# Performance work log

Measured on AMD Instinct MI355X. Metric: run time of the kernel, lower is better.

## Reference

```python
import jax, jax.numpy as jnp
import numpy as np

N, T, H, D = 512, 256, 512, 9  # batch, decode steps, hidden, feature dim


def setup_inputs() -> dict:
    key = jax.random.key(0)
    ks = jax.random.split(key, 4)
    s = 1.0 / np.sqrt(H)
    return {
        "x": jax.random.normal(ks[0], (N, T + 1, D), dtype=jnp.float32),
        "W_ih": jax.random.normal(ks[1], (4 * H, D), dtype=jnp.float32) * s,
        "W_hh": jax.random.normal(ks[2], (4 * H, H), dtype=jnp.float32) * s,
        "b_ih": jnp.zeros((4 * H,), dtype=jnp.float32),
        "b_hh": jnp.zeros((4 * H,), dtype=jnp.float32),
        "fc_W": jax.random.normal(ks[3], (D, H), dtype=jnp.float32) * s,
        "fc_b": jnp.zeros((D,), dtype=jnp.float32),
        "h0": jnp.zeros((1, H), dtype=jnp.float32),
        "c0": jnp.zeros((1, H), dtype=jnp.float32),
    }


def _lstm_cell(x_proj, h, c, W_hh, b_hh):
    # x_proj = x @ W_ih.T + b_ih, precomputed. PyTorch LSTMCell gate order: i, f, g, o
    gates = x_proj + h @ W_hh.T + b_hh
    i, f, g, o = jnp.split(gates, 4, axis=-1)
    c_new = jax.nn.sigmoid(f) * c + jax.nn.sigmoid(i) * jnp.tanh(g)
    h_new = jax.nn.sigmoid(o) * jnp.tanh(c_new)
    return h_new, c_new


def reference(x, W_ih, W_hh, b_ih, b_hh, fc_W, fc_b, h0, c0):
    n = x.shape[0]
    h = jnp.broadcast_to(h0, (n, h0.shape[1]))
    c = jnp.broadcast_to(c0, (n, c0.shape[1]))

    # Encode phase: consume all T+1 input steps (precompute input projections in one GEMM)
    x_proj = jnp.einsum('ntd,gd->tng', x, W_ih) + b_ih  # [T+1, N, 4H]

    def enc_step(carry, xp):
        h, c = carry
        h, c = _lstm_cell(xp, h, c, W_hh, b_hh)
        return (h, c), None

    (h, c), _ = jax.lax.scan(enc_step, (h, c), x_proj)

    # Decode phase: T steps with zero input (input projection reduces to b_ih)
    zero_proj = jnp.broadcast_to(b_ih, (n, b_ih.shape[0]))

    def dec_step(carry, _):
        h, c = carry
        h, c = _lstm_cell(zero_proj, h, c, W_hh, b_hh)
        out = jax.nn.sigmoid(h @ fc_W.T + fc_b)  # [N, D]
        return (h, c), out

    n_dec = x.shape[1] - 1
    _, outs = jax.lax.scan(dec_step, (h, c), None, length=n_dec)  # [T, N, D]
    return jnp.transpose(outs, (1, 0, 2))  # [N, T, D]
```

## Files before the change

### kernel.cpp

```cpp
#include <hip/hip_runtime.h>


#define TT 256
#define HH 512
#define DD 9
#define TP1 257
#define NSTEP 513
#define THREADS 512
#define NWG 256
#define NCL 8
#define WPC 32

#define WF_HI_B 0u
#define WF_LO_B 2097152u
#define HFRAG_B 4194304u
#define U32_B   8388608u

#define L_ST    0
#define L_EX    16384
#define L_HNEW  20480
#define L_WIH   21520
#define L_MISC  22160
#define L_TOT   22164

typedef short s8v __attribute__((ext_vector_type(8)));
typedef float f4v __attribute__((ext_vector_type(4)));
typedef int   i4v __attribute__((ext_vector_type(4)));

__device__ __forceinline__ float sigmoidf_(float v){ return 1.0f/(1.0f+__expf(-v)); }
__device__ __forceinline__ float tanhf_(float v){ return 1.0f - 2.0f/(__expf(2.0f*v)+1.0f); }
__device__ __forceinline__ unsigned short bf16hi_rne(float f){
    unsigned u = __float_as_uint(f);
    return (unsigned short)((u + 0x7fffu + ((u>>16)&1u)) >> 16);
}
#define B2F_LO(u) __uint_as_float(((unsigned)(u))<<16)
#define B2F_HI(u) __uint_as_float(((unsigned)(u)) & 0xffff0000u)

__device__ __forceinline__ void ld16i(i4v& d, const char* p){
    asm volatile("global_load_dwordx4 %0, %1, off sc0" : "=v"(d) : "v"(p));
}
__device__ __forceinline__ void wait_vm0_mem(){
    asm volatile("s_waitcnt vmcnt(0)" ::: "memory");
}
__device__ __forceinline__ void wait_vm0_4i(i4v& a0,i4v& a1,i4v& a2,i4v& a3){
    asm volatile("s_waitcnt vmcnt(0)"
                 : "+v"(a0),"+v"(a1),"+v"(a2),"+v"(a3) :: "memory");
}
__device__ __forceinline__ void lgkm0_bar(){
    asm volatile("s_waitcnt lgkmcnt(0)" ::: "memory");
    __builtin_amdgcn_s_barrier();
}

__global__ void rnn_init_kernel(const float* __restrict__ W_hh,
                                const float* __restrict__ h0,
                                char* __restrict__ wsb) {
    int idx = blockIdx.x * blockDim.x + threadIdx.x;
    {
        int i  = idx & 7;
        int l  = (idx >> 3) & 63;
        int kt = (idx >> 9) & 15;
        int rb = (idx >> 13) & 3;
        int wl = idx >> 15;
        int mm = l & 15, gg = l >> 4;
        int gt = mm & 3, lu = mm >> 2;
        int grow = gt * 512 + wl * 16 + rb * 4 + lu;
        int k = kt * 32 + gg * 8 + i;
        float v = W_hh[grow * 512 + k];
        unsigned short hi = bf16hi_rne(v);
        float fh = __uint_as_float(((unsigned)hi) << 16);
        unsigned short lo = bf16hi_rne(v - fh);
        ((unsigned short*)(wsb + WF_HI_B))[idx] = hi;
        ((unsigned short*)(wsb + WF_LO_B))[idx] = lo;
    }
    if (idx < 262144) {
        int i   = idx & 7;
        int gg  = (idx >> 9) & 3;
        int kt  = (idx >> 11) & 15;
        int cl  = idx >> 15;
        int rem = idx & 32767;
        int j = kt * 32 + gg * 8 + i;
        ((unsigned short*)(wsb + HFRAG_B + (unsigned)cl * 65536u))[rem] = bf16hi_rne(h0[j]);
    }
    if (idx < 2048) ((unsigned int*)(wsb + U32_B))[idx] = 0u;
}

__global__ __attribute__((amdgpu_waves_per_eu(2, 2))) __launch_bounds__(THREADS)
void rnn_persist_kernel(const float* __restrict__ x,
                        const float* __restrict__ W_ih,
                        const float* __restrict__ b_ih,
                        const float* __restrict__ b_hh,
                        const float* __restrict__ fc_W,
                        const float* __restrict__ fc_b,
                        const float* __restrict__ c0,
                        char* __restrict__ wsb,
                        float* __restrict__ out) {
    __shared__ float smem[L_TOT];
    char* ldsst = (char*)smem;

    const int wg  = blockIdx.x;
    const int cl  = wg & 7;
    const int wl  = wg >> 3;
    const int j0  = wl * 16;
    const int nb0 = cl * 64;
    const int tid = threadIdx.x;
    const int lane = tid & 63;
    const int wid  = tid >> 6;
    const int rb   = wid & 3;
    const int kh   = wid >> 2;
    const int m    = lane & 15;
    const int g    = lane >> 4;
    const int gu   = wl * 16 + rb * 4 + g;
    const int c0i  = kh * 32 + m;

    unsigned int* flags = (unsigned int*)(wsb + U32_B);
    unsigned int* ctr   = (unsigned int*)(wsb + U32_B + 3072);
    unsigned int* xccb  = (unsigned int*)(wsb + U32_B + 4096);

    for (int i2 = tid; i2 < 16 * 36; i2 += THREADS) {
        int u = i2 / 36; int r2 = i2 - u * 36; int gt = r2 / 9; int d = r2 - gt * 9;
        smem[L_WIH + u * 40 + gt * 9 + d] = W_ih[(gt * 512 + wl * 16 + u) * DD + d];
    }

    const float bias0 = b_ih[gu]        + b_hh[gu];
    const float bias1 = b_ih[512 + gu]  + b_hh[512 + gu];
    const float bias2 = b_ih[1024 + gu] + b_hh[1024 + gu];
    const float bias3 = b_ih[1536 + gu] + b_hh[1536 + gu];
    float creg0 = c0[gu], creg1 = c0[gu];

    s8v wAh[8], wAl[8];
    {
        const char* base = wsb + (unsigned)(((wl*4 + rb)*16 + kh*8)*64 + lane)*16u;
#pragma unroll
        for (int j = 0; j < 8; ++j) {
            wAh[j] = *(const s8v*)(base + WF_HI_B + j*1024);
            wAl[j] = *(const s8v*)(base + WF_LO_B + j*1024);
        }
    }

    if (tid == 0) {
        unsigned xcc;
        asm volatile("s_getreg_b32 %0, hwreg(HW_REG_XCC_ID, 0, 32)" : "=s"(xcc));
        __hip_atomic_store(xccb + wg, xcc + 1u, __ATOMIC_RELAXED, __HIP_MEMORY_SCOPE_AGENT);
        __hip_atomic_fetch_add(ctr, 1u, __ATOMIC_RELEASE, __HIP_MEMORY_SCOPE_AGENT);
        while (__hip_atomic_load(ctr, __ATOMIC_RELAXED, __HIP_MEMORY_SCOPE_AGENT) < NWG)
            __builtin_amdgcn_s_sleep(8);
    }
    __syncthreads();
    {
        unsigned v = (tid < WPC)
            ? __hip_atomic_load(xccb + cl + 8 * tid, __ATOMIC_RELAXED,
                                __HIP_MEMORY_SCOPE_AGENT) : 0u;
        unsigned v0 = __shfl(v, 0, 64);
        bool ok = (tid >= WPC) || (v != 0u && v == v0);
        unsigned long long mk = __ballot(ok);
        if (tid == 0) smem[L_MISC] = (mk == ~0ull) ? 1.0f : 0.0f;
    }
    __syncthreads();
    const bool fast = (smem[L_MISC] != 0.0f);

    const int fg = tid >> 4, fl = tid & 15;

    for (int s = 0; s < NSTEP; ++s) {
        const int par = s & 1;
        const char* hsrc = wsb + HFRAG_B + (unsigned)(par*8 + cl) * 65536u;
        unsigned int* flg = flags + cl * 32;
        const bool dec = (s >= TP1 + 1);
        const bool enc = (s < TP1);

        if (s > 0) {
            if (tid < WPC) {
                for (;;) {
                    unsigned v = __hip_atomic_load(flg + tid, __ATOMIC_RELAXED,
                                                   __HIP_MEMORY_SCOPE_AGENT);
                    if (__all((int)(v >= (unsigned)s))) break;
                    __builtin_amdgcn_s_sleep(2);
                }
            }
            __syncthreads();
            if (fast) __builtin_amdgcn_fence(__ATOMIC_ACQUIRE, "workgroup");
            else      __builtin_amdgcn_fence(__ATOMIC_ACQUIRE, "agent");
        }

        i4v hb[4];
#pragma unroll
        for (int c = 0; c < 4; ++c)
            ld16i(hb[c], hsrc + c*8192 + tid*16);

        float xv0[DD], xv1[DD];
        if (enc) {
            const float* xp0 = x + (size_t)(nb0 + c0i) * (TP1 * DD) + s * DD;
            const float* xp1 = x + (size_t)(nb0 + c0i + 16) * (TP1 * DD) + s * DD;
#pragma unroll
            for (int d = 0; d < DD; ++d) { xv0[d] = xp0[d]; xv1[d] = xp1[d]; }
        }

        wait_vm0_mem();
#pragma unroll
        for (int c = 0; c < 4; ++c)
            *(i4v*)(ldsst + c*8192 + tid*16) = hb[c];
#pragma unroll
        for (int c = 0; c < 4; ++c)
            ld16i(hb[c], hsrc + 32768 + c*8192 + tid*16);
        lgkm0_bar();

        f4v a0 = {0,0,0,0}, a1 = {0,0,0,0}, a2 = {0,0,0,0}, a3 = {0,0,0,0};
        if (kh == 0) {
#pragma unroll
            for (int j = 0; j < 8; ++j) {
                const char* bb = ldsst + j*4096 + g*1024 + m*16;
                s8v bh0 = *(const s8v*)(bb);
                s8v bh1 = *(const s8v*)(bb + 256);
                s8v bh2 = *(const s8v*)(bb + 512);
                s8v bh3 = *(const s8v*)(bb + 768);
                a0 = __builtin_amdgcn_mfma_f32_16x16x32_bf16(wAh[j], bh0, a0, 0,0,0);
                a1 = __builtin_amdgcn_mfma_f32_16x16x32_bf16(wAh[j], bh1, a1, 0,0,0);
                a2 = __builtin_amdgcn_mfma_f32_16x16x32_bf16(wAh[j], bh2, a2, 0,0,0);
                a3 = __builtin_amdgcn_mfma_f32_16x16x32_bf16(wAh[j], bh3, a3, 0,0,0);
                a0 = __builtin_amdgcn_mfma_f32_16x16x32_bf16(wAl[j], bh0, a0, 0,0,0);
                a1 = __builtin_amdgcn_mfma_f32_16x16x32_bf16(wAl[j], bh1, a1, 0,0,0);
                a2 = __builtin_amdgcn_mfma_f32_16x16x32_bf16(wAl[j], bh2, a2, 0,0,0);
                a3 = __builtin_amdgcn_mfma_f32_16x16x32_bf16(wAl[j], bh3, a3, 0,0,0);
            }
            float* pe = smem + L_EX + ((rb*2 + 0)*64 + lane)*8;
            *(f4v*)(pe)     = a2;
            *(f4v*)(pe + 4) = a3;
        }

        wait_vm0_mem();
#pragma unroll
        for (int c = 0; c < 4; ++c)
            *(i4v*)(ldsst + 32768 + c*8192 + tid*16) = hb[c];

        i4v qa0, qa1, qa2, qa3;
        if (dec) {
            const int bselL = (fg < 2 * DD) ? (fg / DD) : 0;
            const int blL = wl * 2 + bselL;
            const char* hp = hsrc + fl*4096 + blL*16;
            ld16i(qa0, hp);          ld16i(qa1, hp + 1024);
            ld16i(qa2, hp + 2048);   ld16i(qa3, hp + 3072);
        }
        lgkm0_bar();

        if (kh == 1) {
#pragma unroll
            for (int j = 0; j < 8; ++j) {
                const char* bb = ldsst + 32768 + j*4096 + g*1024 + m*16;
                s8v bh0 = *(const s8v*)(bb);
                s8v bh1 = *(const s8v*)(bb + 256);
                s8v bh2 = *(const s8v*)(bb + 512);
                s8v bh3 = *(const s8v*)(bb + 768);
                a0 = __builtin_amdgcn_mfma_f32_16x16x32_bf16(wAh[j], bh0, a0, 0,0,0);
                a1 = __builtin_amdgcn_mfma_f32_16x16x32_bf16(wAh[j], bh1, a1, 0,0,0);
                a2 = __builtin_amdgcn_mfma_f32_16x16x32_bf16(wAh[j], bh2, a2, 0,0,0);
                a3 = __builtin_amdgcn_mfma_f32_16x16x32_bf16(wAh[j], bh3, a3, 0,0,0);
                a0 = __builtin_amdgcn_mfma_f32_16x16x32_bf16(wAl[j], bh0, a0, 0,0,0);
                a1 = __builtin_amdgcn_mfma_f32_16x16x32_bf16(wAl[j], bh1, a1, 0,0,0);
                a2 = __builtin_amdgcn_mfma_f32_16x16x32_bf16(wAl[j], bh2, a2, 0,0,0);
                a3 = __builtin_amdgcn_mfma_f32_16x16x32_bf16(wAl[j], bh3, a3, 0,0,0);
            }
            float* pe = smem + L_EX + ((rb*2 + 1)*64 + lane)*8;
            *(f4v*)(pe)     = a0;
            *(f4v*)(pe + 4) = a1;
        }
        lgkm0_bar();

        {
            const float* px = smem + L_EX + ((rb*2 + (kh^1))*64 + lane)*8;
            f4v r0 = *(const f4v*)(px);
            f4v r1 = *(const f4v*)(px + 4);
            f4v ka, kb;
            if (kh == 0) { ka = a0 + r0; kb = a1 + r1; }
            else         { ka = a2 + r0; kb = a3 + r1; }

            float s00=0,s01=0,s02=0,s03=0, s10=0,s11=0,s12=0,s13=0;
            if (enc) {
                const float* wb2 = smem + L_WIH + (rb*4 + g) * 40;
#pragma unroll
                for (int r2 = 0; r2 < 9; ++r2) {
                    f4v w4 = *(const f4v*)(wb2 + r2*4);
#pragma unroll
                    for (int e = 0; e < 4; ++e) {
                        const int fl2 = r2*4 + e;
                        const int gt = fl2 / 9, d = fl2 - gt*9;
                        const float w = w4[e];
                        const float p0 = xv0[d] * w, p1 = xv1[d] * w;
                        if (gt == 0) { s00 += p0; s10 += p1; }
                        else if (gt == 1) { s01 += p0; s11 += p1; }
                        else if (gt == 2) { s02 += p0; s12 += p1; }
                        else { s03 += p0; s13 += p1; }
                    }
                }
            }
            {
                float vi = ka.x + bias0 + s00, vf = ka.y + bias1 + s01;
                float vg = ka.z + bias2 + s02, vo = ka.w + bias3 + s03;
                float cn = sigmoidf_(vf) * creg0 + sigmoidf_(vi) * tanhf_(vg);
                creg0 = cn;
                smem[L_HNEW + (rb*4 + g) * 65 + c0i] = sigmoidf_(vo) * tanhf_(cn);
            }
            {
                float vi = kb.x + bias0 + s10, vf = kb.y + bias1 + s11;
                float vg = kb.z + bias2 + s12, vo = kb.w + bias3 + s13;
                float cn = sigmoidf_(vf) * creg1 + sigmoidf_(vi) * tanhf_(vg);
                creg1 = cn;
                smem[L_HNEW + (rb*4 + g) * 65 + c0i + 16] = sigmoidf_(vo) * tanhf_(cn);
            }
        }
        lgkm0_bar();

        if (tid < 128) {
            const int col = tid & 63, jblk = (tid >> 6) & 1;
            const int jb = wl * 2 + jblk;
            const int kt = jb >> 2, gg = jb & 3;
            s8v v;
#pragma unroll
            for (int i = 0; i < 8; ++i)
                v[i] = (short)bf16hi_rne(smem[L_HNEW + (jblk * 8 + i) * 65 + col]);
            char* dst = wsb + HFRAG_B + (unsigned)((par^1)*8 + cl)*65536u
                        + (unsigned)(kt*4096 + gg*1024 + col*16);
            *(s8v*)dst = v;
        }
        wait_vm0_mem();
        __syncthreads();

        if (tid == 0) {
            if (fast) {
                __hip_atomic_store(flg + wl, (unsigned)(s + 1),
                                   __ATOMIC_RELAXED, __HIP_MEMORY_SCOPE_AGENT);
            } else {
                __builtin_amdgcn_fence(__ATOMIC_RELEASE, "agent");
                __hip_atomic_store(flg + wl, (unsigned)(s + 1),
                                   __ATOMIC_RELEASE, __HIP_MEMORY_SCOPE_AGENT);
            }
        }

        if (dec && fg < 2 * DD) {
            const int bsel = fg / DD, d = fg - bsel * DD;
            const int bl = wl * 2 + bsel;
            const f4v* wf = (const f4v*)(fc_W + d * HH + fl * 32);
            wait_vm0_4i(qa0, qa1, qa2, qa3);
            float acc = 0.f;
            acc += B2F_LO(qa0.x)*wf[0].x + B2F_HI(qa0.x)*wf[0].y
                 + B2F_LO(qa0.y)*wf[0].z + B2F_HI(qa0.y)*wf[0].w
                 + B2F_LO(qa0.z)*wf[1].x + B2F_HI(qa0.z)*wf[1].y
                 + B2F_LO(qa0.w)*wf[1].z + B2F_HI(qa0.w)*wf[1].w;
            acc += B2F_LO(qa1.x)*wf[2].x + B2F_HI(qa1.x)*wf[2].y
                 + B2F_LO(qa1.y)*wf[2].z + B2F_HI(qa1.y)*wf[2].w
                 + B2F_LO(qa1.z)*wf[3].x + B2F_HI(qa1.z)*wf[3].y
                 + B2F_LO(qa1.w)*wf[3].z + B2F_HI(qa1.w)*wf[3].w;
            acc += B2F_LO(qa2.x)*wf[4].x + B2F_HI(qa2.x)*wf[4].y
                 + B2F_LO(qa2.y)*wf[4].z + B2F_HI(qa2.y)*wf[4].w
                 + B2F_LO(qa2.z)*wf[5].x + B2F_HI(qa2.z)*wf[5].y
                 + B2F_LO(qa2.w)*wf[5].z + B2F_HI(qa2.w)*wf[5].w;
            acc += B2F_LO(qa3.x)*wf[6].x + B2F_HI(qa3.x)*wf[6].y
                 + B2F_LO(qa3.y)*wf[6].z + B2F_HI(qa3.y)*wf[6].w
                 + B2F_LO(qa3.z)*wf[7].x + B2F_HI(qa3.z)*wf[7].y
                 + B2F_LO(qa3.w)*wf[7].z + B2F_HI(qa3.w)*wf[7].w;
            acc += __shfl_down(acc, 8, 16);
            acc += __shfl_down(acc, 4, 16);
            acc += __shfl_down(acc, 2, 16);
            acc += __shfl_down(acc, 1, 16);
            if (fl == 0)
                out[(size_t)(nb0 + bl) * (TT * DD) + (s - (TP1 + 1)) * DD + d] =
                    1.0f / (1.0f + __expf(-(acc + fc_b[d])));
        }
    }

    {
        if (tid < WPC) {
            for (;;) {
                unsigned v = __hip_atomic_load(flags + cl * 32 + tid,
                                               __ATOMIC_RELAXED, __HIP_MEMORY_SCOPE_AGENT);
                if (__all((int)(v >= (unsigned)NSTEP))) break;
                __builtin_amdgcn_s_sleep(2);
            }
        }
        __syncthreads();
        if (fast) __builtin_amdgcn_fence(__ATOMIC_ACQUIRE, "workgroup");
        else      __builtin_amdgcn_fence(__ATOMIC_ACQUIRE, "agent");

        if (fg < 2 * DD) {
            const int bsel = fg / DD, d = fg - bsel * DD;
            const int bl = wl * 2 + bsel;
            const char* hp = wsb + HFRAG_B + (unsigned)((NSTEP & 1)*8 + cl)*65536u
                             + (unsigned)(fl*4096 + bl*16);
            i4v qa0, qa1, qa2, qa3;
            ld16i(qa0, hp);          ld16i(qa1, hp + 1024);
            ld16i(qa2, hp + 2048);   ld16i(qa3, hp + 3072);
            const f4v* wf = (const f4v*)(fc_W + d * HH + fl * 32);
            wait_vm0_4i(qa0, qa1, qa2, qa3);
            float acc = 0.f;
            acc += B2F_LO(qa0.x)*wf[0].x + B2F_HI(qa0.x)*wf[0].y
                 + B2F_LO(qa0.y)*wf[0].z + B2F_HI(qa0.y)*wf[0].w
                 + B2F_LO(qa0.z)*wf[1].x + B2F_HI(qa0.z)*wf[1].y
                 + B2F_LO(qa0.w)*wf[1].z + B2F_HI(qa0.w)*wf[1].w;
            acc += B2F_LO(qa1.x)*wf[2].x + B2F_HI(qa1.x)*wf[2].y
                 + B2F_LO(qa1.y)*wf[2].z + B2F_HI(qa1.y)*wf[2].w
                 + B2F_LO(qa1.z)*wf[3].x + B2F_HI(qa1.z)*wf[3].y
                 + B2F_LO(qa1.w)*wf[3].z + B2F_HI(qa1.w)*wf[3].w;
            acc += B2F_LO(qa2.x)*wf[4].x + B2F_HI(qa2.x)*wf[4].y
                 + B2F_LO(qa2.y)*wf[4].z + B2F_HI(qa2.y)*wf[4].w
                 + B2F_LO(qa2.z)*wf[5].x + B2F_HI(qa2.z)*wf[5].y
                 + B2F_LO(qa2.w)*wf[5].z + B2F_HI(qa2.w)*wf[5].w;
            acc += B2F_LO(qa3.x)*wf[6].x + B2F_HI(qa3.x)*wf[6].y
                 + B2F_LO(qa3.y)*wf[6].z + B2F_HI(qa3.y)*wf[6].w
                 + B2F_LO(qa3.z)*wf[7].x + B2F_HI(qa3.z)*wf[7].y
                 + B2F_LO(qa3.w)*wf[7].z + B2F_HI(qa3.w)*wf[7].w;
            acc += __shfl_down(acc, 8, 16);
            acc += __shfl_down(acc, 4, 16);
            acc += __shfl_down(acc, 2, 16);
            acc += __shfl_down(acc, 1, 16);
            if (fl == 0)
                out[(size_t)(nb0 + bl) * (TT * DD) + 255 * DD + d] =
                    1.0f / (1.0f + __expf(-(acc + fc_b[d])));
        }
    }
}

extern "C" void kernel_launch(void* const* d_in, const int* in_sizes, int n_in,
                              void* d_out, int out_size, void* d_ws, size_t ws_size,
                              hipStream_t stream) {
    (void)in_sizes; (void)n_in; (void)out_size; (void)ws_size;
    const float* x    = (const float*)d_in[0];
    const float* W_ih = (const float*)d_in[1];
    const float* W_hh = (const float*)d_in[2];
    const float* b_ih = (const float*)d_in[3];
    const float* b_hh = (const float*)d_in[4];
    const float* fc_W = (const float*)d_in[5];
    const float* fc_b = (const float*)d_in[6];
    const float* h0   = (const float*)d_in[7];
    const float* c0   = (const float*)d_in[8];
    float* out = (float*)d_out;
    char*  wsb = (char*)d_ws;

    hipLaunchKernelGGL(rnn_init_kernel, dim3(4096), dim3(256), 0, stream,
                       W_hh, h0, wsb);
    hipLaunchKernelGGL(rnn_persist_kernel, dim3(NWG), dim3(THREADS), 0, stream,
                       x, W_ih, b_ih, b_hh, fc_W, fc_b, c0, wsb, out);
}
```

Before: 2.439 ms.

## Load full h fragment at once so both K-halves run MFMAs concurrently

Before, the kh=0 waves ran their MFMA half while the second half of h was still being staged into LDS, and the kh=1 waves waited for it. Now all eight 16-byte h chunks are loaded and written to LDS together, and both K-halves do their MFMAs at the same time, with one barrier removed. The x loads for the encode step are also hoisted above the flag spin-wait, so their latency hides behind the synchronisation. In exchange, each thread holds twice as many h registers, which adds register pressure at two waves per EU, and the earlier global-to-LDS overlap is lost.

```diff
diff --git a/kernel.cpp b/kernel.cpp
--- a/kernel.cpp
+++ b/kernel.cpp
@@ -100,7 +100,6 @@
     const int wg  = blockIdx.x;
     const int cl  = wg & 7;
     const int wl  = wg >> 3;
-    const int j0  = wl * 16;
     const int nb0 = cl * 64;
     const int tid = threadIdx.x;
     const int lane = tid & 63;
@@ -167,6 +166,14 @@
         const bool dec = (s >= TP1 + 1);
         const bool enc = (s < TP1);
 
+        float xv0[DD], xv1[DD];
+        if (enc) {
+            const float* xp0 = x + (size_t)(nb0 + c0i) * (TP1 * DD) + s * DD;
+            const float* xp1 = x + (size_t)(nb0 + c0i + 16) * (TP1 * DD) + s * DD;
+#pragma unroll
+            for (int d = 0; d < DD; ++d) { xv0[d] = xp0[d]; xv1[d] = xp1[d]; }
+        }
+
         if (s > 0) {
             if (tid < WPC) {
                 for (;;) {
@@ -181,33 +188,31 @@
             else      __builtin_amdgcn_fence(__ATOMIC_ACQUIRE, "agent");
         }
 
-        i4v hb[4];
-#pragma unroll
-        for (int c = 0; c < 4; ++c)
+        i4v hb[8];
+#pragma unroll
+        for (int c = 0; c < 8; ++c)
             ld16i(hb[c], hsrc + c*8192 + tid*16);
 
-        float xv0[DD], xv1[DD];
-        if (enc) {
-            const float* xp0 = x + (size_t)(nb0 + c0i) * (TP1 * DD) + s * DD;
-            const float* xp1 = x + (size_t)(nb0 + c0i + 16) * (TP1 * DD) + s * DD;
-#pragma unroll
-            for (int d = 0; d < DD; ++d) { xv0[d] = xp0[d]; xv1[d] = xp1[d]; }
-        }
-
         wait_vm0_mem();
 #pragma unroll
-        for (int c = 0; c < 4; ++c)
+        for (int c = 0; c < 8; ++c)
             *(i4v*)(ldsst + c*8192 + tid*16) = hb[c];
-#pragma unroll
-        for (int c = 0; c < 4; ++c)
-            ld16i(hb[c], hsrc + 32768 + c*8192 + tid*16);
+        i4v qa0, qa1, qa2, qa3;
+        if (dec) {
+            const int bselL = (fg < 2 * DD) ? (fg / DD) : 0;
+            const int blL = wl * 2 + bselL;
+            const char* hp = hsrc + fl*4096 + blL*16;
+            ld16i(qa0, hp);          ld16i(qa1, hp + 1024);
+            ld16i(qa2, hp + 2048);   ld16i(qa3, hp + 3072);
+        }
         lgkm0_bar();
 
         f4v a0 = {0,0,0,0}, a1 = {0,0,0,0}, a2 = {0,0,0,0}, a3 = {0,0,0,0};
-        if (kh == 0) {
+        {
+            const char* base = ldsst + kh*32768;
 #pragma unroll
             for (int j = 0; j < 8; ++j) {
-                const char* bb = ldsst + j*4096 + g*1024 + m*16;
+                const char* bb = base + j*4096 + g*1024 + m*16;
                 s8v bh0 = *(const s8v*)(bb);
                 s8v bh1 = *(const s8v*)(bb + 256);
                 s8v bh2 = *(const s8v*)(bb + 512);
@@ -221,46 +226,9 @@
                 a2 = __builtin_amdgcn_mfma_f32_16x16x32_bf16(wAl[j], bh2, a2, 0,0,0);
                 a3 = __builtin_amdgcn_mfma_f32_16x16x32_bf16(wAl[j], bh3, a3, 0,0,0);
             }
-            float* pe = smem + L_EX + ((rb*2 + 0)*64 + lane)*8;
-            *(f4v*)(pe)     = a2;
-            *(f4v*)(pe + 4) = a3;
-        }
-
-        wait_vm0_mem();
-#pragma unroll
-        for (int c = 0; c < 4; ++c)
-            *(i4v*)(ldsst + 32768 + c*8192 + tid*16) = hb[c];
-
-        i4v qa0, qa1, qa2, qa3;
-        if (dec) {
-            const int bselL = (fg < 2 * DD) ? (fg / DD) : 0;
-            const int blL = wl * 2 + bselL;
-            const char* hp = hsrc + fl*4096 + blL*16;
-            ld16i(qa0, hp);          ld16i(qa1, hp + 1024);
-            ld16i(qa2, hp + 2048);   ld16i(qa3, hp + 3072);
-        }
-        lgkm0_bar();
-
-        if (kh == 1) {
-#pragma unroll
-            for (int j = 0; j < 8; ++j) {
-                const char* bb = ldsst + 32768 + j*4096 + g*1024 + m*16;
-                s8v bh0 = *(const s8v*)(bb);
-                s8v bh1 = *(const s8v*)(bb + 256);
-                s8v bh2 = *(const s8v*)(bb + 512);
-                s8v bh3 = *(const s8v*)(bb + 768);
-                a0 = __builtin_amdgcn_mfma_f32_16x16x32_bf16(wAh[j], bh0, a0, 0,0,0);
-                a1 = __builtin_amdgcn_mfma_f32_16x16x32_bf16(wAh[j], bh1, a1, 0,0,0);
-                a2 = __builtin_amdgcn_mfma_f32_16x16x32_bf16(wAh[j], bh2, a2, 0,0,0);
-                a3 = __builtin_amdgcn_mfma_f32_16x16x32_bf16(wAh[j], bh3, a3, 0,0,0);
-                a0 = __builtin_amdgcn_mfma_f32_16x16x32_bf16(wAl[j], bh0, a0, 0,0,0);
-                a1 = __builtin_amdgcn_mfma_f32_16x16x32_bf16(wAl[j], bh1, a1, 0,0,0);
-                a2 = __builtin_amdgcn_mfma_f32_16x16x32_bf16(wAl[j], bh2, a2, 0,0,0);
-                a3 = __builtin_amdgcn_mfma_f32_16x16x32_bf16(wAl[j], bh3, a3, 0,0,0);
-            }
-            float* pe = smem + L_EX + ((rb*2 + 1)*64 + lane)*8;
-            *(f4v*)(pe)     = a0;
-            *(f4v*)(pe + 4) = a1;
+            float* pe = smem + L_EX + ((rb*2 + kh)*64 + lane)*8;
+            if (kh == 0) { *(f4v*)(pe) = a2; *(f4v*)(pe + 4) = a3; }
+            else         { *(f4v*)(pe) = a0; *(f4v*)(pe + 4) = a1; }
         }
         lgkm0_bar();
 
```

Result: faster. 2.299 ms (-5.8%).
